# Kernel optimization log

Measured on AMD Instinct MI355X. Metric: run time of the kernel, lower is better.

## Reference

```python
import jax, jax.numpy as jnp
import numpy as np

B, S, HIDDEN = 4, 2048, 1024
NUM_EXPERTS = 8
TOP_K = 4
EPS = 1e-6


def setup_inputs() -> dict:
    key = jax.random.key(0)
    k0, k1, k2 = jax.random.split(key, 3)
    x = jax.random.normal(k0, (B, S, HIDDEN), dtype=jnp.float32)
    Wg = jax.random.normal(k1, (HIDDEN, NUM_EXPERTS), dtype=jnp.float32) * 0.02
    bg = jnp.zeros((NUM_EXPERTS,), dtype=jnp.float32)
    W = jax.random.normal(k2, (NUM_EXPERTS, HIDDEN, HIDDEN), dtype=jnp.float32) * 0.02
    b = jnp.zeros((NUM_EXPERTS, HIDDEN), dtype=jnp.float32)
    return {"x": x, "Wg": Wg, "bg": bg, "W": W, "b": b}


def reference(x, Wg, bg, W, b):
    Bb, Ss, D = x.shape
    xf = x.reshape(-1, D)                       # [T, D]
    T = xf.shape[0]

    # --- router ---
    router_logits = xf @ Wg + bg                # [T, E]
    router_probs = jax.nn.softmax(router_logits, axis=-1)
    top_k_probs, top_k_indices = jax.lax.top_k(router_probs, TOP_K)  # [T, K]
    top_k_weights = top_k_probs / (top_k_probs.sum(axis=-1, keepdims=True) + EPS)
    expert_mask = jax.nn.one_hot(top_k_indices, NUM_EXPERTS, dtype=jnp.float32).sum(axis=1)  # [T, E]

    # --- experts: original computes every expert on every token then masks;
    # same math expressed as one batched GEMM + gather ---
    all_out = jnp.einsum('td,edf->etf', xf, W) + b[:, None, :]  # [E, T, D]
    sel = all_out[top_k_indices.T, jnp.arange(T)[None, :]]      # [K, T, D]
    moe_output = jnp.einsum('tk,ktd->td', top_k_weights, sel).reshape(Bb, Ss, D)

    # --- load-balancing aux loss ---
    aux_loss = jnp.dot(expert_mask.mean(axis=0), router_probs.mean(axis=0)) * NUM_EXPERTS
    return moe_output, aux_loss
```

## Files before the change

### kernel.cpp

```cpp
#include <hip/hip_runtime.h>
#include <hip/hip_bf16.h>

#define T_TOK 8192
#define DH    1024
#define NE    8
#define TK    4

typedef unsigned short u16;
typedef __bf16 bf16x8 __attribute__((ext_vector_type(8)));
typedef float  f32x4  __attribute__((ext_vector_type(4)));

__device__ __forceinline__ u16 f2b(float f) {
    union { float f; unsigned u; } v; v.f = f;
    unsigned u = v.u;
    u += 0x7FFFu + ((u >> 16) & 1u);
    return (u16)(u >> 16);
}
__device__ __forceinline__ float b2f(u16 h) {
    union { unsigned u; float f; } v; v.u = ((unsigned)h) << 16;
    return v.f;
}

__global__ __launch_bounds__(256) void cast_x_kernel(const float* __restrict__ x,
                                                     u16* __restrict__ xb) {
    size_t i = ((size_t)blockIdx.x * 256 + threadIdx.x) * 4;
    const float4 v = *(const float4*)(x + i);
    ushort4 o;
    o.x = f2b(v.x); o.y = f2b(v.y); o.z = f2b(v.z); o.w = f2b(v.w);
    *(ushort4*)(xb + i) = o;
}

__global__ __launch_bounds__(256) void cast_w_kernel(const float* __restrict__ W,
                                                     u16* __restrict__ wbt) {
    __shared__ float tile[32][33];
    const int e  = blockIdx.z;
    const int d0 = blockIdx.y * 32;
    const int f0 = blockIdx.x * 32;
    const float* src = W + ((size_t)e << 20);
    for (int r = threadIdx.y; r < 32; r += 8)
        tile[r][threadIdx.x] = src[(size_t)(d0 + r) * DH + f0 + threadIdx.x];
    __syncthreads();
    u16* dst = wbt + ((size_t)e << 20);
    for (int r = threadIdx.y; r < 32; r += 8)
        dst[(size_t)(f0 + r) * DH + d0 + threadIdx.x] = f2b(tile[threadIdx.x][r]);
}

__global__ __launch_bounds__(512) void router_kernel(
    const float* __restrict__ x, const float* __restrict__ Wg, const float* __restrict__ bg,
    int* __restrict__ bucket_tok, float* __restrict__ bucket_w,
    int* __restrict__ tk_e, float* __restrict__ tk_w,
    int* __restrict__ cnt, float* __restrict__ probsum)
{
    __shared__ int   lcnt[NE];
    __shared__ float lprob[NE];
    __shared__ int   gbase[NE];
    const int tid = threadIdx.x;
    const int wv = tid >> 6, lane = tid & 63;
    const int t = blockIdx.x * 8 + wv;
    if (tid < NE) { lcnt[tid] = 0; lprob[tid] = 0.f; }
    __syncthreads();

    float a[NE] = {};
    {
        const float* xr = x + (size_t)t * DH;
        for (int d = lane; d < DH; d += 64) {
            const float xv = xr[d];
            const float* wr = Wg + d * NE;
            #pragma unroll
            for (int e = 0; e < NE; e++) a[e] += xv * wr[e];
        }
    }
    #pragma unroll
    for (int e = 0; e < NE; e++) {
        float v = a[e];
        #pragma unroll
        for (int off = 32; off > 0; off >>= 1) v += __shfl_down(v, off);
        a[e] = v;
    }

    int idx4[TK]; float w4[TK]; int off4[TK];
    if (lane == 0) {
        float logits[NE], probs[NE];
        float mx = -1e30f;
        #pragma unroll
        for (int e = 0; e < NE; e++) { logits[e] = a[e] + bg[e]; mx = fmaxf(mx, logits[e]); }
        float Z = 0.f;
        #pragma unroll
        for (int e = 0; e < NE; e++) { probs[e] = expf(logits[e] - mx); Z += probs[e]; }
        const float rZ = 1.f / Z;
        #pragma unroll
        for (int e = 0; e < NE; e++) probs[e] *= rZ;

        float rem[NE];
        #pragma unroll
        for (int e = 0; e < NE; e++) rem[e] = probs[e];
        float s4 = 0.f;
        #pragma unroll
        for (int k = 0; k < TK; k++) {
            int best = 0; float bv = rem[0];
            #pragma unroll
            for (int e = 1; e < NE; e++) if (rem[e] > bv) { bv = rem[e]; best = e; }
            idx4[k] = best; w4[k] = bv; s4 += bv; rem[best] = -1e30f;
        }
        const float rs = 1.f / (s4 + 1e-6f);
        #pragma unroll
        for (int k = 0; k < TK; k++) {
            w4[k] *= rs;
            tk_e[t * TK + k] = idx4[k];
            tk_w[t * TK + k] = w4[k];
            off4[k] = atomicAdd(&lcnt[idx4[k]], 1);
        }
        #pragma unroll
        for (int e = 0; e < NE; e++) atomicAdd(&lprob[e], probs[e]);
    }
    __syncthreads();
    if (tid < NE) {
        gbase[tid] = atomicAdd(&cnt[tid], lcnt[tid]);
        atomicAdd(&probsum[tid], lprob[tid]);
    }
    __syncthreads();
    if (lane == 0) {
        #pragma unroll
        for (int k = 0; k < TK; k++) {
            const int e = idx4[k];
            const int slot = gbase[e] + off4[k];
            bucket_tok[e * T_TOK + slot] = (t << 2) | k;
            bucket_w[e * T_TOK + slot]   = w4[k];
        }
    }
}

__global__ void aux_kernel(const int* __restrict__ cnt, const float* __restrict__ probsum,
                           float* __restrict__ out_aux) {
    if (threadIdx.x == 0 && blockIdx.x == 0) {
        float s = 0.f;
        for (int e = 0; e < NE; e++) s += (float)cnt[e] * probsum[e];
        out_aux[0] = s * (float)NE / ((float)T_TOK * (float)T_TOK);
    }
}

__global__ __launch_bounds__(256) void moe_gemm_kernel(
    const u16* __restrict__ xb, const u16* __restrict__ wbt,
    const int* __restrict__ bucket_tok, const float* __restrict__ bucket_w,
    const int* __restrict__ cnt, u16* __restrict__ y)
{
    const int e  = blockIdx.z;
    const int M  = cnt[e];
    const int m0 = blockIdx.y * 128;
    if (m0 >= M) return;
    const int n0 = blockIdx.x * 128;

    __shared__ u16 As[128 * 40];
    __shared__ u16 Bs[128 * 40];
    __shared__ int   s_tok[128];
    __shared__ float s_w[128];

    const int tid  = threadIdx.x;
    const int lane = tid & 63;
    const int wave = tid >> 6;

    if (tid < 128) {
        const int slot = m0 + tid;
        if (slot < M) {
            s_tok[tid] = bucket_tok[e * T_TOK + slot];
            s_w[tid]   = bucket_w[e * T_TOK + slot];
        } else { s_tok[tid] = -1; s_w[tid] = 0.f; }
    }
    __syncthreads();

    const int rA = tid >> 2;
    const int cA = (tid & 3) * 8;
    const int tokA1 = s_tok[rA];
    const int tokA2 = s_tok[64 + rA];
    const u16* a1 = xb + (size_t)((tokA1 >= 0) ? (tokA1 >> 2) : 0) * DH + cA;
    const u16* a2 = xb + (size_t)((tokA2 >= 0) ? (tokA2 >> 2) : 0) * DH + cA;
    const u16* b1 = wbt + ((size_t)e << 20) + (size_t)(n0 + rA) * DH + cA;
    const u16* b2 = b1 + (size_t)64 * DH;

    u16* A1d = &As[rA * 40 + cA];
    u16* A2d = &As[(64 + rA) * 40 + cA];
    u16* B1d = &Bs[rA * 40 + cA];
    u16* B2d = &Bs[(64 + rA) * 40 + cA];

    const int mrow = (wave >> 1) * 64;
    const int ncol = (wave & 1) * 64;
    const int fr   = lane & 15;
    const int fq   = (lane >> 4) * 8;

    f32x4 acc[4][4] = {};

    for (int k0 = 0; k0 < DH; k0 += 32) {
        *(bf16x8*)A1d = *(const bf16x8*)(a1 + k0);
        *(bf16x8*)A2d = *(const bf16x8*)(a2 + k0);
        *(bf16x8*)B1d = *(const bf16x8*)(b1 + k0);
        *(bf16x8*)B2d = *(const bf16x8*)(b2 + k0);
        __syncthreads();
        bf16x8 af[4], bfv[4];
        #pragma unroll
        for (int i = 0; i < 4; i++)
            af[i] = *(const bf16x8*)&As[(mrow + i * 16 + fr) * 40 + fq];
        #pragma unroll
        for (int j = 0; j < 4; j++)
            bfv[j] = *(const bf16x8*)&Bs[(ncol + j * 16 + fr) * 40 + fq];
        #pragma unroll
        for (int i = 0; i < 4; i++)
            #pragma unroll
            for (int j = 0; j < 4; j++)
                acc[i][j] = __builtin_amdgcn_mfma_f32_16x16x32_bf16(af[i], bfv[j], acc[i][j], 0, 0, 0);
        __syncthreads();
    }

    const int cl = lane & 15;
    const int rb = (lane >> 4) * 4;
    #pragma unroll
    for (int i = 0; i < 4; i++) {
        #pragma unroll
        for (int r = 0; r < 4; r++) {
            const int srow = mrow + i * 16 + rb + r;
            const int tok = s_tok[srow];
            if (tok < 0) continue;
            const float w = s_w[srow];
            u16* yr = y + (size_t)tok * DH + (n0 + ncol + cl);
            #pragma unroll
            for (int j = 0; j < 4; j++)
                yr[j * 16] = f2b(acc[i][j][r] * w);
        }
    }
}

__global__ __launch_bounds__(256) void combine_kernel(
    const u16* __restrict__ y, const int* __restrict__ tk_e, const float* __restrict__ tk_w,
    const float* __restrict__ bexp, float* __restrict__ out)
{
    const int t = blockIdx.x;
    const int c = threadIdx.x * 4;
    float o0 = 0.f, o1 = 0.f, o2 = 0.f, o3 = 0.f;
    #pragma unroll
    for (int k = 0; k < TK; k++) {
        const int e   = tk_e[t * TK + k];
        const float w = tk_w[t * TK + k];
        const ushort4 yv = *(const ushort4*)(y + ((size_t)(t * TK + k)) * DH + c);
        const float4  bv = *(const float4*)(bexp + (size_t)e * DH + c);
        o0 += b2f(yv.x) + w * bv.x;
        o1 += b2f(yv.y) + w * bv.y;
        o2 += b2f(yv.z) + w * bv.z;
        o3 += b2f(yv.w) + w * bv.w;
    }
    float4 ov = {o0, o1, o2, o3};
    *(float4*)(out + (size_t)t * DH + c) = ov;
}

extern "C" void kernel_launch(void* const* d_in, const int* in_sizes, int n_in,
                              void* d_out, int out_size, void* d_ws, size_t ws_size,
                              hipStream_t stream)
{
    const float* x  = (const float*)d_in[0];
    const float* Wg = (const float*)d_in[1];
    const float* bg = (const float*)d_in[2];
    const float* W  = (const float*)d_in[3];
    const float* b  = (const float*)d_in[4];
    float* out = (float*)d_out;

    char* ws = (char*)d_ws;
    u16*   xb         = (u16*)(ws);
    u16*   wbt        = (u16*)(ws + 16777216);
    u16*   y          = (u16*)(ws + 33554432);
    int*   bucket_tok = (int*)(ws + 100663296);
    float* bucket_w   = (float*)(ws + 100925440);
    int*   tk_e       = (int*)(ws + 101187584);
    float* tk_w       = (float*)(ws + 101318656);
    int*   cnt        = (int*)(ws + 101449728);
    float* probsum    = (float*)(ws + 101449760);

    hipMemsetAsync(cnt, 0, 64, stream);

    cast_x_kernel<<<8192, 256, 0, stream>>>(x, xb);
    cast_w_kernel<<<dim3(32, 32, NE), dim3(32, 8, 1), 0, stream>>>(W, wbt);
    router_kernel<<<1024, 512, 0, stream>>>(x, Wg, bg, bucket_tok, bucket_w, tk_e, tk_w, cnt, probsum);
    aux_kernel<<<1, 64, 0, stream>>>(cnt, probsum, out + (size_t)T_TOK * DH);
    moe_gemm_kernel<<<dim3(8, 64, NE), 256, 0, stream>>>(xb, wbt, bucket_tok, bucket_w, cnt, y);
    combine_kernel<<<8192, 256, 0, stream>>>(y, tk_e, tk_w, b, out);
}
```

Before: 285.0 us.

## Fuse x cast into router, fold aux into combine, use direct-to-LDS loads

The bf16 cast of x moves into the router kernel, which already reads x, so one full pass over x and one launch go away. The aux-loss computation folds into combine_kernel to save another launch. The GEMM tile loads now use global_load_lds to go straight to LDS without passing through registers, and the LDS padding is removed to fit that layout. Dropping the padding may add bank conflicts on the MFMA fragment reads, and the router now does more memory work per wave.

```diff
diff --git a/kernel.cpp b/kernel.cpp
--- a/kernel.cpp
+++ b/kernel.cpp
@@ -20,14 +20,9 @@
     union { unsigned u; float f; } v; v.u = ((unsigned)h) << 16;
     return v.f;
 }
-
-__global__ __launch_bounds__(256) void cast_x_kernel(const float* __restrict__ x,
-                                                     u16* __restrict__ xb) {
-    size_t i = ((size_t)blockIdx.x * 256 + threadIdx.x) * 4;
-    const float4 v = *(const float4*)(x + i);
-    ushort4 o;
-    o.x = f2b(v.x); o.y = f2b(v.y); o.z = f2b(v.z); o.w = f2b(v.w);
-    *(ushort4*)(xb + i) = o;
+__device__ __forceinline__ void glds16(const u16* g, u16* l) {
+    __builtin_amdgcn_global_load_lds((const __attribute__((address_space(1))) void*)g,
+                                     (__attribute__((address_space(3))) void*)l, 16, 0, 0);
 }
 
 __global__ __launch_bounds__(256) void cast_w_kernel(const float* __restrict__ W,
@@ -47,6 +42,7 @@
 
 __global__ __launch_bounds__(512) void router_kernel(
     const float* __restrict__ x, const float* __restrict__ Wg, const float* __restrict__ bg,
+    u16* __restrict__ xb,
     int* __restrict__ bucket_tok, float* __restrict__ bucket_w,
     int* __restrict__ tk_e, float* __restrict__ tk_w,
     int* __restrict__ cnt, float* __restrict__ probsum)
@@ -63,11 +59,18 @@
     float a[NE] = {};
     {
         const float* xr = x + (size_t)t * DH;
-        for (int d = lane; d < DH; d += 64) {
-            const float xv = xr[d];
+        u16* xbr = xb + (size_t)t * DH;
+        #pragma unroll
+        for (int it = 0; it < 4; it++) {
+            const int d = it * 256 + lane * 4;
+            const float4 v = *(const float4*)(xr + d);
+            ushort4 o;
+            o.x = f2b(v.x); o.y = f2b(v.y); o.z = f2b(v.z); o.w = f2b(v.w);
+            *(ushort4*)(xbr + d) = o;
             const float* wr = Wg + d * NE;
             #pragma unroll
-            for (int e = 0; e < NE; e++) a[e] += xv * wr[e];
+            for (int e = 0; e < NE; e++)
+                a[e] += v.x * wr[e] + v.y * wr[NE + e] + v.z * wr[2 * NE + e] + v.w * wr[3 * NE + e];
         }
     }
     #pragma unroll
@@ -130,15 +133,6 @@
     }
 }
 
-__global__ void aux_kernel(const int* __restrict__ cnt, const float* __restrict__ probsum,
-                           float* __restrict__ out_aux) {
-    if (threadIdx.x == 0 && blockIdx.x == 0) {
-        float s = 0.f;
-        for (int e = 0; e < NE; e++) s += (float)cnt[e] * probsum[e];
-        out_aux[0] = s * (float)NE / ((float)T_TOK * (float)T_TOK);
-    }
-}
-
 __global__ __launch_bounds__(256) void moe_gemm_kernel(
     const u16* __restrict__ xb, const u16* __restrict__ wbt,
     const int* __restrict__ bucket_tok, const float* __restrict__ bucket_w,
@@ -150,8 +144,8 @@
     if (m0 >= M) return;
     const int n0 = blockIdx.x * 128;
 
-    __shared__ u16 As[128 * 40];
-    __shared__ u16 Bs[128 * 40];
+    __shared__ u16 As[128 * 32];
+    __shared__ u16 Bs[128 * 32];
     __shared__ int   s_tok[128];
     __shared__ float s_w[128];
 
@@ -168,19 +162,19 @@
     }
     __syncthreads();
 
-    const int rA = tid >> 2;
-    const int cA = (tid & 3) * 8;
-    const int tokA1 = s_tok[rA];
-    const int tokA2 = s_tok[64 + rA];
-    const u16* a1 = xb + (size_t)((tokA1 >= 0) ? (tokA1 >> 2) : 0) * DH + cA;
-    const u16* a2 = xb + (size_t)((tokA2 >= 0) ? (tokA2 >> 2) : 0) * DH + cA;
-    const u16* b1 = wbt + ((size_t)e << 20) + (size_t)(n0 + rA) * DH + cA;
-    const u16* b2 = b1 + (size_t)64 * DH;
-
-    u16* A1d = &As[rA * 40 + cA];
-    u16* A2d = &As[(64 + rA) * 40 + cA];
-    u16* B1d = &Bs[rA * 40 + cA];
-    u16* B2d = &Bs[(64 + rA) * 40 + cA];
+    const int l4 = lane >> 2;
+    const int c8 = (lane & 3) * 8;
+    const int r0 = (2 * wave) * 16 + l4;
+    const int r1 = r0 + 16;
+    const int t0 = s_tok[r0], t1 = s_tok[r1];
+    const u16* gA0 = xb + (size_t)(t0 >= 0 ? (t0 >> 2) : 0) * DH + c8;
+    const u16* gA1 = xb + (size_t)(t1 >= 0 ? (t1 >> 2) : 0) * DH + c8;
+    const u16* gB0 = wbt + ((size_t)e << 20) + (size_t)(n0 + r0) * DH + c8;
+    const u16* gB1 = gB0 + (size_t)16 * DH;
+    u16* lA0 = &As[(2 * wave)     * 512];
+    u16* lA1 = &As[(2 * wave + 1) * 512];
+    u16* lB0 = &Bs[(2 * wave)     * 512];
+    u16* lB1 = &Bs[(2 * wave + 1) * 512];
 
     const int mrow = (wave >> 1) * 64;
     const int ncol = (wave & 1) * 64;
@@ -190,18 +184,18 @@
     f32x4 acc[4][4] = {};
 
     for (int k0 = 0; k0 < DH; k0 += 32) {
-        *(bf16x8*)A1d = *(const bf16x8*)(a1 + k0);
-        *(bf16x8*)A2d = *(const bf16x8*)(a2 + k0);
-        *(bf16x8*)B1d = *(const bf16x8*)(b1 + k0);
-        *(bf16x8*)B2d = *(const bf16x8*)(b2 + k0);
+        glds16(gA0 + k0, lA0);
+        glds16(gA1 + k0, lA1);
+        glds16(gB0 + k0, lB0);
+        glds16(gB1 + k0, lB1);
         __syncthreads();
         bf16x8 af[4], bfv[4];
         #pragma unroll
         for (int i = 0; i < 4; i++)
-            af[i] = *(const bf16x8*)&As[(mrow + i * 16 + fr) * 40 + fq];
+            af[i] = *(const bf16x8*)&As[(mrow + i * 16 + fr) * 32 + fq];
         #pragma unroll
         for (int j = 0; j < 4; j++)
-            bfv[j] = *(const bf16x8*)&Bs[(ncol + j * 16 + fr) * 40 + fq];
+            bfv[j] = *(const bf16x8*)&Bs[(ncol + j * 16 + fr) * 32 + fq];
         #pragma unroll
         for (int i = 0; i < 4; i++)
             #pragma unroll
@@ -230,10 +224,17 @@
 
 __global__ __launch_bounds__(256) void combine_kernel(
     const u16* __restrict__ y, const int* __restrict__ tk_e, const float* __restrict__ tk_w,
-    const float* __restrict__ bexp, float* __restrict__ out)
+    const float* __restrict__ bexp,
+    const int* __restrict__ cnt, const float* __restrict__ probsum,
+    float* __restrict__ out, float* __restrict__ out_aux)
 {
     const int t = blockIdx.x;
     const int c = threadIdx.x * 4;
+    if (t == 0 && threadIdx.x == 0) {
+        float s = 0.f;
+        for (int e = 0; e < NE; e++) s += (float)cnt[e] * probsum[e];
+        out_aux[0] = s * (float)NE / ((float)T_TOK * (float)T_TOK);
+    }
     float o0 = 0.f, o1 = 0.f, o2 = 0.f, o3 = 0.f;
     #pragma unroll
     for (int k = 0; k < TK; k++) {
@@ -274,10 +275,8 @@
 
     hipMemsetAsync(cnt, 0, 64, stream);
 
-    cast_x_kernel<<<8192, 256, 0, stream>>>(x, xb);
     cast_w_kernel<<<dim3(32, 32, NE), dim3(32, 8, 1), 0, stream>>>(W, wbt);
-    router_kernel<<<1024, 512, 0, stream>>>(x, Wg, bg, bucket_tok, bucket_w, tk_e, tk_w, cnt, probsum);
-    aux_kernel<<<1, 64, 0, stream>>>(cnt, probsum, out + (size_t)T_TOK * DH);
+    router_kernel<<<1024, 512, 0, stream>>>(x, Wg, bg, xb, bucket_tok, bucket_w, tk_e, tk_w, cnt, probsum);
     moe_gemm_kernel<<<dim3(8, 64, NE), 256, 0, stream>>>(xb, wbt, bucket_tok, bucket_w, cnt, y);
-    combine_kernel<<<8192, 256, 0, stream>>>(y, tk_e, tk_w, b, out);
-}
+    combine_kernel<<<8192, 256, 0, stream>>>(y, tk_e, tk_w, b, cnt, probsum, out, out + (size_t)T_TOK * DH);
+}
```

After: 262.7 us. 7.8% less time.
